# Optimization experiments

Measured on AMD Instinct MI355X. Metric: run time of the kernel, lower is better.

The kernel has to match this reference:

```python
import jax, jax.numpy as jnp
import numpy as np
from jax import lax


def ternarize(w):
    """Standard TWN ternarization with straight-through estimator.
    delta = 0.7*mean(|w|); alpha = mean(|w|) over kept entries; w_t = alpha*sign(w)*mask.
    """
    a = jnp.abs(w)
    delta = 0.7 * a.mean()
    mask = (a > delta).astype(w.dtype)
    alpha = (a * mask).sum() / jnp.maximum(mask.sum(), 1.0)
    wt = alpha * jnp.sign(w) * mask
    return w + lax.stop_gradient(wt - w)  # STE


def conv3x3(x, w, b):
    y = lax.conv_general_dilated(x, ternarize(w), window_strides=(1, 1),
                                 padding=((1, 1), (1, 1)),
                                 dimension_numbers=('NCHW', 'OIHW', 'NCHW'))
    return y + b[None, :, None, None]


def maxpool2(x):
    return lax.reduce_window(x, -jnp.inf, lax.max, (1, 1, 2, 2), (1, 1, 2, 2), 'VALID')


def setup_inputs() -> dict:
    key = jax.random.key(0)
    ks = jax.random.split(key, 11)
    s = lambda k, shape, scale: jax.random.normal(k, shape, dtype=jnp.float32) * scale
    return {
        'x':   s(ks[0], (1024, 3, 32, 32), 1.0),
        'w1':  s(ks[1], (64, 3, 3, 3), 0.1),
        'b1':  s(ks[2], (64,), 0.01),
        'w2':  s(ks[3], (128, 64, 3, 3), 0.05),
        'b2':  s(ks[4], (128,), 0.01),
        'w3':  s(ks[5], (256, 128, 3, 3), 0.03),
        'b3':  s(ks[6], (256,), 0.01),
        'wf1': s(ks[7], (256, 4096), 0.02),
        'bf1': s(ks[8], (256,), 0.01),
        'wf2': s(ks[9], (10, 256), 0.06),
        'bf2': s(ks[10], (10,), 0.01),
    }


def reference(x, w1, b1, w2, b2, w3, b3, wf1, bf1, wf2, bf2):
    x = maxpool2(jax.nn.relu(conv3x3(x, w1, b1)))   # [B,64,16,16]
    x = maxpool2(jax.nn.relu(conv3x3(x, w2, b2)))   # [B,128,8,8]
    x = maxpool2(jax.nn.relu(conv3x3(x, w3, b3)))   # [B,256,4,4]
    x = x.reshape(-1, 256 * 4 * 4)
    x = jax.nn.relu(x @ ternarize(wf1).T + bf1)     # [B,256]
    return x @ ternarize(wf2).T + bf2               # [B,10]
```

## Files before the change

### kernel.cpp

```cpp
#include <hip/hip_runtime.h>
#include <hip/hip_bf16.h>


typedef __attribute__((ext_vector_type(8))) short short8;
typedef __attribute__((ext_vector_type(4))) float f32x4;
typedef __attribute__((ext_vector_type(4))) int i32x4;

#define GLOAD_LDS16(g, l)                                              \
    __builtin_amdgcn_global_load_lds(                                  \
        (const __attribute__((address_space(1))) void*)(g),            \
        (__attribute__((address_space(3))) void*)(l), 16, 0, 0)

__device__ __forceinline__ unsigned short f2bf(float x) {
    unsigned u = __float_as_uint(x);
    return (unsigned short)((u + 0x7fffu + ((u >> 16) & 1u)) >> 16);
}
__device__ __forceinline__ float bf2f(unsigned short b) {
    return __uint_as_float(((unsigned)b) << 16);
}

#define WS_W1B   0
#define N_W1B    2048
#define WS_W2P   (WS_W1B + N_W1B)
#define N_W2P    (9*128*64)
#define WS_W3P   (WS_W2P + N_W2P)
#define N_W3P    (9*256*128)
#define WS_WTF1  (WS_W3P + N_W3P)
#define N_WTF1   (256*4096)
#define WS_WTF2  (WS_WTF1 + N_WTF1)
#define N_WTF2   (10*256)
#define WS_A1    (WS_WTF2 + N_WTF2)
#define N_A1     (1024*256*64)
#define WS_A2    (WS_A1 + N_A1)
#define N_A2     (1024*64*128)
#define WS_A3    (WS_A2 + N_A2)
#define N_A3     (1024*16*256)
#define WS_F1    (WS_A3 + N_A3)
#define N_F1     (1024*256)
#define WS_SCR   (WS_F1 + N_F1)

#define FC1_S    16

struct TernArgs {
    const float* w[6];
    int n[6];
};

__global__ void tern_stats1(TernArgs ta, double* __restrict__ scr) {
    const int wi = blockIdx.y;
    const float* __restrict__ w = ta.w[wi];
    const int n = ta.n[wi];
    __shared__ double red[4];
    const int lane = threadIdx.x & 63, wv = threadIdx.x >> 6;
    if (wi == 5) {
        float m = 0.f;
        for (int i = blockIdx.x * blockDim.x + threadIdx.x; i < n;
             i += gridDim.x * blockDim.x)
            m = fmaxf(m, fabsf(w[i]));
        #pragma unroll
        for (int off = 32; off > 0; off >>= 1)
            m = fmaxf(m, __shfl_down(m, off, 64));
        if (lane == 0) red[wv] = (double)m;
        __syncthreads();
        if (threadIdx.x == 0) {
            float mm = (float)fmax(fmax(red[0], red[1]), fmax(red[2], red[3]));
            atomicMax((int*)(scr + 20), __float_as_int(mm));
        }
        return;
    }
    double s = 0.0;
    for (int i = blockIdx.x * blockDim.x + threadIdx.x; i < n;
         i += gridDim.x * blockDim.x)
        s += (double)fabsf(w[i]);
    #pragma unroll
    for (int off = 32; off > 0; off >>= 1) s += __shfl_down(s, off, 64);
    if (lane == 0) red[wv] = s;
    __syncthreads();
    if (threadIdx.x == 0)
        atomicAdd(scr + wi * 4, red[0] + red[1] + red[2] + red[3]);
}

__global__ void tern_stats2(TernArgs ta, double* __restrict__ scr) {
    const int wi = blockIdx.y;
    const float* __restrict__ w = ta.w[wi];
    const int n = ta.n[wi];
    const float delta = (float)(0.7 * scr[wi * 4] / (double)n);
    double ms = 0.0, cnt = 0.0;
    for (int i = blockIdx.x * blockDim.x + threadIdx.x; i < n;
         i += gridDim.x * blockDim.x) {
        float a = fabsf(w[i]);
        if (a > delta) { ms += (double)a; cnt += 1.0; }
    }
    #pragma unroll
    for (int off = 32; off > 0; off >>= 1) {
        ms += __shfl_down(ms, off, 64);
        cnt += __shfl_down(cnt, off, 64);
    }
    __shared__ double redm[4], redc[4];
    const int lane = threadIdx.x & 63, wv = threadIdx.x >> 6;
    if (lane == 0) { redm[wv] = ms; redc[wv] = cnt; }
    __syncthreads();
    if (threadIdx.x == 0) {
        atomicAdd(scr + wi * 4 + 1, redm[0] + redm[1] + redm[2] + redm[3]);
        atomicAdd(scr + wi * 4 + 2, redc[0] + redc[1] + redc[2] + redc[3]);
    }
}

__global__ void tern_write_all(TernArgs ta, const double* __restrict__ scr,
                               signed char* __restrict__ w1b,
                               signed char* __restrict__ w2p8,
                               signed char* __restrict__ w3p8,
                               unsigned short* __restrict__ wtf1b,
                               float* __restrict__ wtf2) {
    const int wi = blockIdx.y;
    const float* __restrict__ w = ta.w[wi];
    const int n = ta.n[wi];
    const double* sc = scr + wi * 4;
    const float delta = (float)(0.7 * sc[0] / (double)n);
    const int i0 = blockIdx.x * blockDim.x + threadIdx.x;
    const int stride = gridDim.x * blockDim.x;

    if (wi == 0) {
        for (int i = i0; i < n; i += stride) {
            const int co = i / 27;
            const int kp = i % 27;
            float v = w[i];
            signed char s = (fabsf(v) > delta) ? (v > 0.0f ? 1 : -1) : 0;
            w1b[co * 64 + kp] = s;
            w1b[4096 + co * 64 + 32 + kp] = s;
        }
    } else if (wi == 4) {
        const double c = sc[2];
        const float alpha = (float)(sc[1] / (c > 1.0 ? c : 1.0));
        for (int i = i0; i < n; i += stride) {
            float v = w[i];
            wtf2[i] = (fabsf(v) > delta) ? (v > 0.0f ? alpha : -alpha) : 0.0f;
        }
    } else if (wi == 1 || wi == 2) {
        const int CIc = (wi == 1) ? 64 : 128;
        const int COc = (wi == 1) ? 128 : 256;
        signed char* dst = (wi == 1) ? w2p8 : w3p8;
        for (int i = i0; i < n; i += stride) {
            const int co = i / (CIc * 9);
            const int r = i % (CIc * 9);
            const int ci = r / 9, tap = r % 9;
            float v = w[i];
            signed char s = (fabsf(v) > delta) ? (v > 0.0f ? 1 : -1) : 0;
            dst[(tap * COc + co) * CIc + ci] = s;
        }
    } else {
        for (int i = i0; i < n; i += stride) {
            const int j = i >> 12;
            const int k = i & 4095;
            const int c = k >> 4, px = k & 15;
            float v = w[i];
            unsigned short s = (fabsf(v) > delta) ? (v > 0.0f ? 0x3f80 : 0xbf80) : 0;
            unsigned short* row = wtf1b + ((long)j << 13) + px * 512 + c;
            row[0] = s;
            row[256] = s;
        }
    }
}

__global__ __launch_bounds__(256) void conv1_i8(
        const float* __restrict__ x,
        const signed char* __restrict__ w1b,
        const float* __restrict__ bias,
        const double* __restrict__ scr,
        const int* __restrict__ amax_x,
        int* __restrict__ amax_out,
        float* __restrict__ y) {
    constexpr int PL = 3472;
    __shared__ __align__(16) char X[2 * PL];
    __shared__ float redm[4];

    const int b = blockIdx.x;
    const int tid = threadIdx.x;
    const float S = 32512.0f / fmaxf(__int_as_float(*amax_x), 1e-30f);

    for (int i = tid; i < 2 * PL / 16; i += 256)
        ((int4*)X)[i] = make_int4(0, 0, 0, 0);
    __syncthreads();

    for (int i = tid; i < 768; i += 256) {
        const float4 v = ((const float4*)(x + (long)b * 3072))[i];
        const int e = i * 4;
        const int ci = e >> 10;
        const int rem = e & 1023;
        const int h = rem >> 5, w = rem & 31;
        const int base = ci * 1156 + (h + 1) * 34 + (w + 1);
        const float f[4] = {v.x, v.y, v.z, v.w};
        #pragma unroll
        for (int j = 0; j < 4; j++) {
            const int q = __float2int_rn(f[j] * S);
            const int ql = (q << 24) >> 24;
            const int qh = (q - ql) >> 8;
            X[base + j] = (char)ql;
            X[PL + base + j] = (char)qh;
        }
    }
    __syncthreads();

    const int lane = tid & 63;
    const int wid = tid >> 6;
    const int lm = lane & 15;
    const int kg = lane >> 4;

    const int poff = (kg >= 2) ? PL : 0;
    int cst[16];
    #pragma unroll
    for (int j = 0; j < 16; j++) {
        const int kp = (kg & 1) * 16 + j;
        cst[j] = (kp < 27)
                     ? ((kp / 9) * 1156 + ((kp % 9) / 3) * 34 + (kp % 9) % 3)
                     : 0;
    }

    i32x4 BL[4], BH[4];
    #pragma unroll
    for (int nt = 0; nt < 4; nt++) {
        const int co = nt * 16 + lm;
        BL[nt] = *(const i32x4*)(w1b + (long)co * 64 + kg * 16);
        BH[nt] = *(const i32x4*)(w1b + 4096 + (long)co * 64 + kg * 16);
    }

    const double c2 = scr[2];
    const float alpha = (float)(scr[1] / (c2 > 1.0 ? c2 : 1.0));
    const float dq = alpha / S;
    float tmax = 0.f;
    float* yb = y + (long)b * 256 * 64;

    for (int tt = 0; tt < 16; ++tt) {
        const int t = wid * 16 + tt;
        const int pp = t * 4 + (lm >> 2);
        const int sub = lm & 3;
        const int h = 2 * (pp >> 4) + (sub >> 1);
        const int w = 2 * (pp & 15) + (sub & 1);
        const int base = poff + h * 34 + w;
        unsigned d[4] = {0u, 0u, 0u, 0u};
        #pragma unroll
        for (int j = 0; j < 16; j++) {
            const unsigned byte = (unsigned char)X[base + cst[j]];
            d[j >> 2] |= byte << ((j & 3) * 8);
        }
        i32x4 Af;
        Af[0] = (int)d[0]; Af[1] = (int)d[1];
        Af[2] = (int)d[2]; Af[3] = (int)d[3];

        const int opp = t * 4 + kg;
        float* yr = yb + (long)opp * 64;
        #pragma unroll
        for (int nt = 0; nt < 4; nt++) {
            i32x4 aL = 0, aH = 0;
            aL = __builtin_amdgcn_mfma_i32_16x16x64_i8(Af, BL[nt], aL, 0, 0, 0);
            aH = __builtin_amdgcn_mfma_i32_16x16x64_i8(Af, BH[nt], aH, 0, 0, 0);
            const int s0 = aH[0] * 256 + aL[0];
            const int s1 = aH[1] * 256 + aL[1];
            const int s2 = aH[2] * 256 + aL[2];
            const int s3 = aH[3] * 256 + aL[3];
            int sm = s0 > s1 ? s0 : s1;
            const int sn = s2 > s3 ? s2 : s3;
            sm = sm > sn ? sm : sn;
            const int co = nt * 16 + lm;
            const float o = fmaxf(dq * (float)sm + bias[co], 0.f);
            tmax = fmaxf(tmax, o);
            yr[co] = o;
        }
    }

    #pragma unroll
    for (int off = 32; off > 0; off >>= 1)
        tmax = fmaxf(tmax, __shfl_down(tmax, off, 64));
    if (lane == 0) redm[wid] = tmax;
    __syncthreads();
    if (tid == 0) {
        float m = fmaxf(fmaxf(redm[0], redm[1]), fmaxf(redm[2], redm[3]));
        atomicMax(amax_out, __float_as_int(m));
    }
}

template <int CI, int HI, int CO, int HB, int WM, int WN, bool INF32, int NPH>
__global__ __launch_bounds__(256, 2) void conv_i8(
        const void* __restrict__ xin,
        const signed char* __restrict__ wp,
        const float* __restrict__ bias,
        const double* __restrict__ scr,
        const int* __restrict__ amax_in,
        int* __restrict__ amax_out,
        unsigned short* __restrict__ yout) {
    constexpr int CH8 = CI / 64;
    constexpr int NITER = 9 * CH8;
    constexpr int HR = HI / HB;
    constexpr int ROWS = HR + 2;
    constexpr int COLS = HI + 2;
    constexpr int NPIX = ROWS * COLS;
    constexpr int PSTR = NPIX * 64 + 32;
    constexpr int PO = HI / 2;
    constexpr int POR = HR / 2;
    constexpr int MT = 4, NT = 4;
    constexpr int RWB = HI * CI * 4;
    constexpr int RR = (ROWS + NPH - 1) / NPH;
    static_assert(WM * WN == 4, "4 waves");
    static_assert(WM * 64 == HR * HI, "M covers slab pixels");
    static_assert(WN * 64 == CO, "N covers all co");
    static_assert(RWB == 4096, "row must be 4096 B");

    __shared__ __align__(16) char X[2 * CH8 * PSTR];
    __shared__ __align__(16) char RAW[RR * RWB];
    __shared__ float redm[4];

    const int bimg = blockIdx.x / HB;
    const int hb = blockIdx.x % HB;
    const int tid = threadIdx.x;
    const int lane = tid & 63;
    const int wid = tid >> 6;

    const float S = 32512.0f / fmaxf(__int_as_float(*amax_in), 1e-30f);

    constexpr int HALO = 2 * COLS + 2 * (ROWS - 2);
    for (int i = tid; i < HALO * 2 * CH8 * 4; i += 256) {
        const int u = i & 3;
        const int t = i >> 2;
        const int g = t % (2 * CH8);
        const int hp = t / (2 * CH8);
        int p;
        if (hp < COLS) p = hp;
        else if (hp < 2 * COLS) p = (ROWS - 1) * COLS + (hp - COLS);
        else {
            const int e = hp - 2 * COLS;
            p = (1 + (e >> 1)) * COLS + ((e & 1) ? (COLS - 1) : 0);
        }
        *(int4*)&X[g * PSTR + p * 64 + u * 16] = make_int4(0, 0, 0, 0);
    }

    for (int ph = 0; ph < NPH; ph++) {
        const int r0 = ph * RR;
        const int rend = (r0 + RR < ROWS) ? (r0 + RR) : ROWS;
        for (int r = r0; r < rend; r++) {
            const int h = hb * HR + r - 1;
            const int rl = r - r0;
            if ((unsigned)h >= (unsigned)HI) {
                *(int4*)&RAW[rl * RWB + tid * 16] = make_int4(0, 0, 0, 0);
            } else if (wid == (r & 3)) {
                const char* grow = (const char*)xin +
                                   ((long)(bimg * HI + h)) * RWB;
                #pragma unroll
                for (int j = 0; j < RWB / 1024; j++)
                    GLOAD_LDS16(grow + j * 1024 + lane * 16,
                                &RAW[rl * RWB + j * 1024]);
            }
        }
        __syncthreads();

        const int NIT = (rend - r0) * HI * (CI / 8);
        for (int i = tid; i < NIT; i += 256) {
            const int q8 = i % (CI / 8);
            const int t = i / (CI / 8);
            const int c = t % HI;
            const int rl = t / HI;
            const int r = r0 + rl;
            float f[8];
            if (INF32) {
                const float* pf =
                    (const float*)&RAW[rl * RWB + c * (CI * 4) + q8 * 32];
                const float4 va = *(const float4*)(pf);
                const float4 vb = *(const float4*)(pf + 4);
                f[0] = va.x; f[1] = va.y; f[2] = va.z; f[3] = va.w;
                f[4] = vb.x; f[5] = vb.y; f[6] = vb.z; f[7] = vb.w;
            } else {
                const uint4 vh =
                    *(const uint4*)&RAW[rl * RWB + c * (CI * 4) + q8 * 16];
                const uint4 vl =
                    *(const uint4*)&RAW[rl * RWB + c * (CI * 4) + CI * 2 +
                                        q8 * 16];
                const unsigned* hw = (const unsigned*)&vh;
                const unsigned* lw = (const unsigned*)&vl;
                #pragma unroll
                for (int j = 0; j < 8; j++) {
                    const unsigned hu = (j & 1) ? (hw[j >> 1] >> 16)
                                                : (hw[j >> 1] & 0xffffu);
                    const unsigned lu = (j & 1) ? (lw[j >> 1] >> 16)
                                                : (lw[j >> 1] & 0xffffu);
                    f[j] = __uint_as_float(hu << 16) +
                           __uint_as_float(lu << 16);
                }
            }
            unsigned pl0 = 0, pl1 = 0, ph0 = 0, ph1 = 0;
            #pragma unroll
            for (int j = 0; j < 8; j++) {
                const int qi = (int)(f[j] * S + 0.5f);
                const int ql = (qi << 24) >> 24;
                const int qh = (qi - ql) >> 8;
                const int sh = (j & 3) * 8;
                if (j < 4) {
                    pl0 |= (unsigned)(ql & 255) << sh;
                    ph0 |= (unsigned)(qh & 255) << sh;
                } else {
                    pl1 |= (unsigned)(ql & 255) << sh;
                    ph1 |= (unsigned)(qh & 255) << sh;
                }
            }
            const int p = r * COLS + c + 1;
            const int ch = q8 / (64 / 8);
            const int cc = (q8 * 8) & 63;
            const int slot = ((cc >> 4) + (p >> 1)) & 3;
            const int base = p * 64 + slot * 16 + (cc & 15);
            *(uint2*)&X[ch * PSTR + base] = make_uint2(pl0, pl1);
            *(uint2*)&X[(CH8 + ch) * PSTR + base] = make_uint2(ph0, ph1);
        }
        __syncthreads();
    }

    const int wm = (WM == 1) ? 0 : (wid >> 1);
    const int wn = (WM == 1) ? wid : (wid & 1);
    const int lm = lane & 15;
    const int kg = lane >> 4;

    int pb[MT];
    #pragma unroll
    for (int mt = 0; mt < MT; mt++) {
        const int m = (wm * MT + mt) * 16 + lm;
        const int pp = m >> 2, sub = m & 3;
        const int lph = pp / PO, lpw = pp % PO;
        const int h = 2 * lph + (sub >> 1);
        const int w = 2 * lpw + (sub & 1);
        pb[mt] = h * COLS + w;
    }
    const signed char* bp[NT];
    #pragma unroll
    for (int nt = 0; nt < NT; nt++) {
        const int co = (wn * NT + nt) * 16 + lm;
        bp[nt] = wp + (long)co * CI + kg * 16;
    }

    i32x4 accL[MT][NT], accH[MT][NT];
    #pragma unroll
    for (int mt = 0; mt < MT; mt++)
        #pragma unroll
        for (int nt = 0; nt < NT; nt++) { accL[mt][nt] = 0; accH[mt][nt] = 0; }

    i32x4 Bb[2][NT];
    #pragma unroll
    for (int nt = 0; nt < NT; nt++) Bb[0][nt] = *(const i32x4*)(bp[nt]);

    #pragma unroll 2
    for (int it = 0; it < NITER; ++it) {
        const int cur = it & 1, nxt = cur ^ 1;
        if (it + 1 < NITER) {
            const int it1 = it + 1;
            const int tap = it1 / CH8, ch1 = it1 % CH8;
            const int woff = tap * CO * CI + ch1 * 64;
            #pragma unroll
            for (int nt = 0; nt < NT; nt++)
                Bb[nxt][nt] = *(const i32x4*)(bp[nt] + woff);
        }
        const int tap = it / CH8, ch = it % CH8;
        const int dtap = (tap / 3) * COLS + (tap % 3);
        int ao[MT];
        #pragma unroll
        for (int mt = 0; mt < MT; mt++) {
            const int p = pb[mt] + dtap;
            ao[mt] = p * 64 + (((kg + (p >> 1)) & 3) << 4);
        }
        {
            i32x4 Af[MT];
            #pragma unroll
            for (int mt = 0; mt < MT; mt++)
                Af[mt] = *(const i32x4*)&X[ch * PSTR + ao[mt]];
            #pragma unroll
            for (int mt = 0; mt < MT; mt++)
                #pragma unroll
                for (int nt = 0; nt < NT; nt++)
                    accL[mt][nt] = __builtin_amdgcn_mfma_i32_16x16x64_i8(
                        Af[mt], Bb[cur][nt], accL[mt][nt], 0, 0, 0);
        }
        {
            i32x4 Af[MT];
            #pragma unroll
            for (int mt = 0; mt < MT; mt++)
                Af[mt] = *(const i32x4*)&X[(CH8 + ch) * PSTR + ao[mt]];
            #pragma unroll
            for (int mt = 0; mt < MT; mt++)
                #pragma unroll
                for (int nt = 0; nt < NT; nt++)
                    accH[mt][nt] = __builtin_amdgcn_mfma_i32_16x16x64_i8(
                        Af[mt], Bb[cur][nt], accH[mt][nt], 0, 0, 0);
        }
    }

    const double c2 = scr[2];
    const float alpha = (float)(scr[1] / (c2 > 1.0 ? c2 : 1.0));
    const float dq = alpha / S;
    float tmax = 0.f;
    #pragma unroll
    for (int mt = 0; mt < MT; mt++) {
        const int pp = (wm * MT + mt) * 4 + kg;
        const int lph = pp / PO, lpw = pp % PO;
        const int gpp = (hb * POR + lph) * PO + lpw;
        unsigned short* yr = yout + ((long)bimg * (PO * PO) + gpp) * (2 * CO);
        #pragma unroll
        for (int nt = 0; nt < NT; nt++) {
            const int co = (wn * NT + nt) * 16 + lm;
            const i32x4 aL = accL[mt][nt], aH = accH[mt][nt];
            int s0 = aH[0] * 256 + aL[0];
            int s1 = aH[1] * 256 + aL[1];
            int s2 = aH[2] * 256 + aL[2];
            int s3 = aH[3] * 256 + aL[3];
            int sm = s0 > s1 ? s0 : s1;
            int sn = s2 > s3 ? s2 : s3;
            sm = sm > sn ? sm : sn;
            float o = fmaxf(dq * (float)sm + bias[co], 0.f);
            tmax = fmaxf(tmax, o);
            unsigned short hi = f2bf(o);
            unsigned short lo = f2bf(o - bf2f(hi));
            yr[co] = hi;
            yr[CO + co] = lo;
        }
    }
    if (amax_out) {
        #pragma unroll
        for (int off = 32; off > 0; off >>= 1)
            tmax = fmaxf(tmax, __shfl_down(tmax, off, 64));
        if (lane == 0) redm[wid] = tmax;
        __syncthreads();
        if (tid == 0) {
            float m = fmaxf(fmaxf(redm[0], redm[1]), fmaxf(redm[2], redm[3]));
            atomicMax(amax_out, __float_as_int(m));
        }
    }
}

template <int S>
__global__ __launch_bounds__(256) void fc1_mfma(
        const unsigned short* __restrict__ A,
        const unsigned short* __restrict__ Bw,
        float* __restrict__ parts) {
    constexpr int KCH = 8192 / S;
    constexpr int NSTEP = KCH / 32;
    const int m0 = blockIdx.x * 128;
    const int n0 = blockIdx.y * 128;
    const int s = blockIdx.z;
    const int tid = threadIdx.x;
    const int lane = tid & 63, wid = tid >> 6;
    const int wm = wid >> 1, wn = wid & 1;
    const int lm = lane & 15, kg = lane >> 4;

    const long k0 = (long)s * KCH + kg * 8;
    const unsigned short* ap[4];
    const unsigned short* bp[4];
    #pragma unroll
    for (int t = 0; t < 4; t++) {
        ap[t] = A + (long)(m0 + wm * 64 + t * 16 + lm) * 8192 + k0;
        bp[t] = Bw + (long)(n0 + wn * 64 + t * 16 + lm) * 8192 + k0;
    }

    f32x4 acc[4][4] = {};
    short8 Ab[2][4], Bb[2][4];
    #pragma unroll
    for (int t = 0; t < 4; t++) {
        Ab[0][t] = *(const short8*)(ap[t]);
        Bb[0][t] = *(const short8*)(bp[t]);
    }

    #pragma unroll 2
    for (int st = 0; st < NSTEP; ++st) {
        const int cur = st & 1, nxt = cur ^ 1;
        if (st + 1 < NSTEP) {
            const int off = (st + 1) * 32;
            #pragma unroll
            for (int t = 0; t < 4; t++) {
                Ab[nxt][t] = *(const short8*)(ap[t] + off);
                Bb[nxt][t] = *(const short8*)(bp[t] + off);
            }
        }
        #pragma unroll
        for (int mt = 0; mt < 4; mt++)
            #pragma unroll
            for (int nt = 0; nt < 4; nt++)
                acc[mt][nt] = __builtin_amdgcn_mfma_f32_16x16x32_bf16(
                    Ab[cur][mt], Bb[cur][nt], acc[mt][nt], 0, 0, 0);
    }

    #pragma unroll
    for (int mt = 0; mt < 4; mt++) {
        #pragma unroll
        for (int r = 0; r < 4; r++) {
            const int b = m0 + wm * 64 + mt * 16 + kg * 4 + r;
            #pragma unroll
            for (int nt = 0; nt < 4; nt++) {
                const int j = n0 + wn * 64 + nt * 16 + lm;
                parts[((long)s * 1024 + b) * 256 + j] = acc[mt][nt][r];
            }
        }
    }
}

template <int S>
__global__ __launch_bounds__(256) void fc2_fused(
        const float* __restrict__ parts,
        const double* __restrict__ scr,
        const float* __restrict__ bf1v,
        const float* __restrict__ wtf2,
        const float* __restrict__ bf2v,
        float* __restrict__ out) {
    __shared__ float sf[256];
    const int b = blockIdx.x;
    const int j = threadIdx.x;
    float s = 0.f;
    #pragma unroll
    for (int p = 0; p < S; p++)
        s += parts[(long)p * 262144 + (long)b * 256 + j];
    const double c2 = scr[2];
    const float alpha = (float)(scr[1] / (c2 > 1.0 ? c2 : 1.0));
    sf[j] = fmaxf(alpha * s + bf1v[j], 0.f);
    __syncthreads();
    const int lane = threadIdx.x & 63, wid = threadIdx.x >> 6;
    for (int k = wid; k < 10; k += 4) {
        const float* wr = wtf2 + k * 256;
        float acc = 0.f;
        #pragma unroll
        for (int t = 0; t < 4; t++)
            acc += sf[lane + t * 64] * wr[lane + t * 64];
        #pragma unroll
        for (int off = 32; off > 0; off >>= 1)
            acc += __shfl_down(acc, off, 64);
        if (lane == 0) out[(long)b * 10 + k] = acc + bf2v[k];
    }
}

extern "C" void kernel_launch(void* const* d_in, const int* in_sizes, int n_in,
                              void* d_out, int out_size, void* d_ws, size_t ws_size,
                              hipStream_t stream) {
    const float* x   = (const float*)d_in[0];
    const float* w1  = (const float*)d_in[1];
    const float* b1  = (const float*)d_in[2];
    const float* w2  = (const float*)d_in[3];
    const float* b2  = (const float*)d_in[4];
    const float* w3  = (const float*)d_in[5];
    const float* b3  = (const float*)d_in[6];
    const float* wf1 = (const float*)d_in[7];
    const float* bf1 = (const float*)d_in[8];
    const float* wf2 = (const float*)d_in[9];
    const float* bf2 = (const float*)d_in[10];
    float* out = (float*)d_out;
    float* ws = (float*)d_ws;

    const int B = 1024;

    signed char*    w1b   = (signed char*)(ws + WS_W1B);
    signed char*    w2p8  = (signed char*)(ws + WS_W2P);
    signed char*    w3p8  = (signed char*)(ws + WS_W3P);
    unsigned short* wtf1b = (unsigned short*)(ws + WS_WTF1);
    float*          wtf2  = ws + WS_WTF2;
    float*          a1f   = ws + WS_A1;
    unsigned short* a2p   = (unsigned short*)(ws + WS_A2);
    unsigned short* a3p   = (unsigned short*)(ws + WS_A3);
    double*         scr   = (double*)(ws + WS_SCR);
    int*            iscr  = (int*)(scr + 20);
    int*            amaxx = iscr;
    int*            amax1 = iscr + 1;
    int*            amax2 = iscr + 2;
    float*          parts = ws + WS_A1;

    hipMemsetAsync(scr, 0, 22 * sizeof(double), stream);
    hipMemsetAsync(w1b, 0, 8192, stream);

    TernArgs ta;
    ta.w[0] = w1;  ta.n[0] = 64 * 27;
    ta.w[1] = w2;  ta.n[1] = 128 * 64 * 9;
    ta.w[2] = w3;  ta.n[2] = 256 * 128 * 9;
    ta.w[3] = wf1; ta.n[3] = 256 * 4096;
    ta.w[4] = wf2; ta.n[4] = 10 * 256;
    ta.w[5] = x;   ta.n[5] = 1024 * 3 * 32 * 32;

    hipLaunchKernelGGL(tern_stats1, dim3(128, 6), dim3(256), 0, stream, ta, scr);
    hipLaunchKernelGGL(tern_stats2, dim3(128, 5), dim3(256), 0, stream, ta, scr);
    hipLaunchKernelGGL(tern_write_all, dim3(128, 5), dim3(256), 0, stream,
                       ta, scr, w1b, w2p8, w3p8, wtf1b, wtf2);

    hipLaunchKernelGGL(conv1_i8, dim3(B), dim3(256), 0, stream,
                       x, w1b, b1, scr + 0, amaxx, amax1, a1f);

    hipLaunchKernelGGL((conv_i8<64, 16, 128, 2, 2, 2, true, 1>), dim3(B * 2),
                       dim3(256), 0, stream, a1f, w2p8, b2, scr + 4, amax1,
                       amax2, a2p);

    hipLaunchKernelGGL((conv_i8<128, 8, 256, 1, 1, 4, false, 2>), dim3(B),
                       dim3(256), 0, stream, a2p, w3p8, b3, scr + 8, amax2,
                       (int*)nullptr, a3p);

    hipLaunchKernelGGL((fc1_mfma<FC1_S>), dim3(8, 2, FC1_S), dim3(256), 0, stream,
                       a3p, wtf1b, parts);

    hipLaunchKernelGGL((fc2_fused<FC1_S>), dim3(B), dim3(256), 0, stream,
                       parts, scr + 12, bf1, wtf2, bf2, out);
}
```

Measured before the change: 283.8 us.

## Load only valid halo rows once, overlap with halo zeroing, change swizzle

Drops the phased raw-row staging (NPH) and loads only the in-image rows into a compacted LDS buffer in one pass. The global-to-LDS loads are issued before the halo zero-fill so the two can overlap. The conversion of the fp32 input now works on 4 values at a time, and the high byte is computed with a simpler rounding expression. The swizzle slot is rewritten from row and column parity, with the A-fragment address math precomputed per tile. This removes a barrier and the zeroing of out-of-image rows, but it changes the swizzle formula and uses more LDS for RAW in conv3, which could lower occupancy.

Result: no change. 280.6 us (-1.1%).

```diff
diff --git a/kernel.cpp b/kernel.cpp
--- a/kernel.cpp
+++ b/kernel.cpp
@@ -279,7 +279,7 @@
     }
 }
 
-template <int CI, int HI, int CO, int HB, int WM, int WN, bool INF32, int NPH>
+template <int CI, int HI, int CO, int HB, int WM, int WN, bool INF32>
 __global__ __launch_bounds__(256, 2) void conv_i8(
         const void* __restrict__ xin,
         const signed char* __restrict__ wp,
@@ -299,14 +299,16 @@
     constexpr int POR = HR / 2;
     constexpr int MT = 4, NT = 4;
     constexpr int RWB = HI * CI * 4;
-    constexpr int RR = (ROWS + NPH - 1) / NPH;
+    constexpr int RAWR = (HB == 1) ? (ROWS - 2) : (ROWS - 1);
     static_assert(WM * WN == 4, "4 waves");
     static_assert(WM * 64 == HR * HI, "M covers slab pixels");
     static_assert(WN * 64 == CO, "N covers all co");
     static_assert(RWB == 4096, "row must be 4096 B");
+    static_assert(HB <= 2, "row compaction assumes <=1 invalid row per end");
+    static_assert((COLS & 1) == 0, "swizzle parity uses even COLS");
 
     __shared__ __align__(16) char X[2 * CH8 * PSTR];
-    __shared__ __align__(16) char RAW[RR * RWB];
+    __shared__ __align__(16) char RAW[RAWR * RWB];
     __shared__ float redm[4];
 
     const int bimg = blockIdx.x / HB;
@@ -316,6 +318,21 @@
     const int wid = tid >> 6;
 
     const float S = 32512.0f / fmaxf(__int_as_float(*amax_in), 1e-30f);
+
+    const int rlo = (hb == 0) ? 1 : 0;
+    const int rhi = (hb == HB - 1) ? (ROWS - 1) : ROWS;
+    for (int r = rlo; r < rhi; r++) {
+        if (wid == (r & 3)) {
+            const int h = hb * HR + r - 1;
+            const int rl = r - rlo;
+            const char* grow = (const char*)xin +
+                               ((long)(bimg * HI + h)) * RWB;
+            #pragma unroll
+            for (int j = 0; j < RWB / 1024; j++)
+                GLOAD_LDS16(grow + j * 1024 + lane * 16,
+                            &RAW[rl * RWB + j * 1024]);
+        }
+    }
 
     constexpr int HALO = 2 * COLS + 2 * (ROWS - 2);
     for (int i = tid; i < HALO * 2 * CH8 * 4; i += 256) {
@@ -332,91 +349,86 @@
         }
         *(int4*)&X[g * PSTR + p * 64 + u * 16] = make_int4(0, 0, 0, 0);
     }
-
-    for (int ph = 0; ph < NPH; ph++) {
-        const int r0 = ph * RR;
-        const int rend = (r0 + RR < ROWS) ? (r0 + RR) : ROWS;
-        for (int r = r0; r < rend; r++) {
-            const int h = hb * HR + r - 1;
-            const int rl = r - r0;
-            if ((unsigned)h >= (unsigned)HI) {
-                *(int4*)&RAW[rl * RWB + tid * 16] = make_int4(0, 0, 0, 0);
-            } else if (wid == (r & 3)) {
-                const char* grow = (const char*)xin +
-                                   ((long)(bimg * HI + h)) * RWB;
-                #pragma unroll
-                for (int j = 0; j < RWB / 1024; j++)
-                    GLOAD_LDS16(grow + j * 1024 + lane * 16,
-                                &RAW[rl * RWB + j * 1024]);
+    __syncthreads();
+
+    if (INF32) {
+        constexpr int NIT = RAWR * HI * (CI / 4);
+        for (int i = tid; i < NIT; i += 256) {
+            const int q4 = i % (CI / 4);
+            const int t = i / (CI / 4);
+            const int c = t % HI;
+            const int rl = t / HI;
+            const int r = rlo + rl;
+            const float4 v =
+                *(const float4*)&RAW[rl * RWB + c * (CI * 4) + q4 * 16];
+            const float f[4] = {v.x, v.y, v.z, v.w};
+            unsigned pl = 0, ph = 0;
+            #pragma unroll
+            for (int j = 0; j < 4; j++) {
+                const int qi = (int)(f[j] * S + 0.5f);
+                pl |= (unsigned)(qi & 255) << (j * 8);
+                ph |= (unsigned)(((qi + 128) >> 8) & 255) << (j * 8);
             }
-        }
-        __syncthreads();
-
-        const int NIT = (rend - r0) * HI * (CI / 8);
+            const int p = r * COLS + c + 1;
+            const int cc = (q4 * 4) & 63;
+            const int ch = q4 / 16;
+            const int slot = ((cc >> 4) + ((c + 1) >> 1) + 2 * r) & 3;
+            const int base = p * 64 + slot * 16 + (cc & 15);
+            *(unsigned*)&X[ch * PSTR + base] = pl;
+            *(unsigned*)&X[(CH8 + ch) * PSTR + base] = ph;
+        }
+    } else {
+        constexpr int NIT = RAWR * HI * (CI / 8);
         for (int i = tid; i < NIT; i += 256) {
             const int q8 = i % (CI / 8);
             const int t = i / (CI / 8);
             const int c = t % HI;
             const int rl = t / HI;
-            const int r = r0 + rl;
+            const int r = rlo + rl;
+            const uint4 vh =
+                *(const uint4*)&RAW[rl * RWB + c * (CI * 4) + q8 * 16];
+            const uint4 vl =
+                *(const uint4*)&RAW[rl * RWB + c * (CI * 4) + CI * 2 +
+                                    q8 * 16];
+            const unsigned* hw = (const unsigned*)&vh;
+            const unsigned* lw = (const unsigned*)&vl;
             float f[8];
-            if (INF32) {
-                const float* pf =
-                    (const float*)&RAW[rl * RWB + c * (CI * 4) + q8 * 32];
-                const float4 va = *(const float4*)(pf);
-                const float4 vb = *(const float4*)(pf + 4);
-                f[0] = va.x; f[1] = va.y; f[2] = va.z; f[3] = va.w;
-                f[4] = vb.x; f[5] = vb.y; f[6] = vb.z; f[7] = vb.w;
-            } else {
-                const uint4 vh =
-                    *(const uint4*)&RAW[rl * RWB + c * (CI * 4) + q8 * 16];
-                const uint4 vl =
-                    *(const uint4*)&RAW[rl * RWB + c * (CI * 4) + CI * 2 +
-                                        q8 * 16];
-                const unsigned* hw = (const unsigned*)&vh;
-                const unsigned* lw = (const unsigned*)&vl;
-                #pragma unroll
-                for (int j = 0; j < 8; j++) {
-                    const unsigned hu = (j & 1) ? (hw[j >> 1] >> 16)
-                                                : (hw[j >> 1] & 0xffffu);
-                    const unsigned lu = (j & 1) ? (lw[j >> 1] >> 16)
-                                                : (lw[j >> 1] & 0xffffu);
-                    f[j] = __uint_as_float(hu << 16) +
-                           __uint_as_float(lu << 16);
-                }
+            #pragma unroll
+            for (int j = 0; j < 8; j++) {
+                const unsigned hu = (j & 1) ? (hw[j >> 1] >> 16)
+                                            : (hw[j >> 1] & 0xffffu);
+                const unsigned lu = (j & 1) ? (lw[j >> 1] >> 16)
+                                            : (lw[j >> 1] & 0xffffu);
+                f[j] = __uint_as_float(hu << 16) + __uint_as_float(lu << 16);
             }
             unsigned pl0 = 0, pl1 = 0, ph0 = 0, ph1 = 0;
             #pragma unroll
             for (int j = 0; j < 8; j++) {
                 const int qi = (int)(f[j] * S + 0.5f);
-                const int ql = (qi << 24) >> 24;
-                const int qh = (qi - ql) >> 8;
                 const int sh = (j & 3) * 8;
-                if (j < 4) {
-                    pl0 |= (unsigned)(ql & 255) << sh;
-                    ph0 |= (unsigned)(qh & 255) << sh;
-                } else {
-                    pl1 |= (unsigned)(ql & 255) << sh;
-                    ph1 |= (unsigned)(qh & 255) << sh;
-                }
+                const unsigned lb = (unsigned)(qi & 255) << sh;
+                const unsigned hbyte =
+                    (unsigned)(((qi + 128) >> 8) & 255) << sh;
+                if (j < 4) { pl0 |= lb; ph0 |= hbyte; }
+                else       { pl1 |= lb; ph1 |= hbyte; }
             }
             const int p = r * COLS + c + 1;
-            const int ch = q8 / (64 / 8);
+            const int ch = q8 / 8;
             const int cc = (q8 * 8) & 63;
-            const int slot = ((cc >> 4) + (p >> 1)) & 3;
+            const int slot = ((cc >> 4) + ((c + 1) >> 1) + 2 * r) & 3;
             const int base = p * 64 + slot * 16 + (cc & 15);
             *(uint2*)&X[ch * PSTR + base] = make_uint2(pl0, pl1);
             *(uint2*)&X[(CH8 + ch) * PSTR + base] = make_uint2(ph0, ph1);
         }
-        __syncthreads();
-    }
+    }
+    __syncthreads();
 
     const int wm = (WM == 1) ? 0 : (wid >> 1);
     const int wn = (WM == 1) ? wid : (wid & 1);
     const int lm = lane & 15;
     const int kg = lane >> 4;
 
-    int pb[MT];
+    int pq[MT];
     #pragma unroll
     for (int mt = 0; mt < MT; mt++) {
         const int m = (wm * MT + mt) * 16 + lm;
@@ -424,7 +436,7 @@
         const int lph = pp / PO, lpw = pp % PO;
         const int h = 2 * lph + (sub >> 1);
         const int w = 2 * lpw + (sub & 1);
-        pb[mt] = h * COLS + w;
+        pq[mt] = ((h * COLS + w) << 6) | ((h & 1) << 3) | (w & 7);
     }
     const signed char* bp[NT];
     #pragma unroll
@@ -455,12 +467,16 @@
                 Bb[nxt][nt] = *(const i32x4*)(bp[nt] + woff);
         }
         const int tap = it / CH8, ch = it % CH8;
-        const int dtap = (tap / 3) * COLS + (tap % 3);
+        const int ty = tap / 3, tx = tap % 3;
+        const int DT = (ty * COLS + tx) << 6;
+        const int typ = ty & 1;
         int ao[MT];
         #pragma unroll
         for (int mt = 0; mt < MT; mt++) {
-            const int p = pb[mt] + dtap;
-            ao[mt] = p * 64 + (((kg + (p >> 1)) & 3) << 4);
+            const int q = pq[mt];
+            const int slot = (kg + ((((q >> 3) & 1) + typ) & 1) * 2 +
+                              (((q & 7) + tx) >> 1)) & 3;
+            ao[mt] = (q & ~63) + DT + (slot << 4);
         }
         {
             i32x4 Af[MT];
@@ -681,11 +697,11 @@
     hipLaunchKernelGGL(conv1_i8, dim3(B), dim3(256), 0, stream,
                        x, w1b, b1, scr + 0, amaxx, amax1, a1f);
 
-    hipLaunchKernelGGL((conv_i8<64, 16, 128, 2, 2, 2, true, 1>), dim3(B * 2),
+    hipLaunchKernelGGL((conv_i8<64, 16, 128, 2, 2, 2, true>), dim3(B * 2),
                        dim3(256), 0, stream, a1f, w2p8, b2, scr + 4, amax1,
                        amax2, a2p);
 
-    hipLaunchKernelGGL((conv_i8<128, 8, 256, 1, 1, 4, false, 2>), dim3(B),
+    hipLaunchKernelGGL((conv_i8<128, 8, 256, 1, 1, 4, false>), dim3(B),
                        dim3(256), 0, stream, a2p, w3p8, b3, scr + 8, amax2,
                        (int*)nullptr, a3p);
 
```
